# Kernel optimization log

Hardware: AMD Instinct MI355X
Metric: run time of the kernel (lower is better)

Reference implementation:

```python
import jax, jax.numpy as jnp
import numpy as np

B, S, D = 2, 2048, 768
H, DK, DV = 12, 64, 64


def setup_inputs() -> dict:
    key = jax.random.key(0)
    ks = jax.random.split(key, 12)
    sc = 0.02
    return {
        'q': jax.random.normal(ks[0], (B, S, D), jnp.float32),
        'k': jax.random.normal(ks[1], (B, S, D), jnp.float32),
        'v': jax.random.normal(ks[2], (B, S, D), jnp.float32),
        'mask': jnp.zeros((B, H, S, S), jnp.float32),
        'Wq': jax.random.normal(ks[3], (D, H * DK), jnp.float32) * sc,
        'bq': jnp.zeros((H * DK,), jnp.float32),
        'Wk': jax.random.normal(ks[4], (D, H * DK), jnp.float32) * sc,
        'bk': jnp.zeros((H * DK,), jnp.float32),
        'Wv': jax.random.normal(ks[5], (D, H * DV), jnp.float32) * sc,
        'bv': jnp.zeros((H * DV,), jnp.float32),
        'Wo': jax.random.normal(ks[6], (H * DV, D), jnp.float32) * sc,
        'bo': jnp.zeros((D,), jnp.float32),
    }


def reference(q, k, v, mask, Wq, bq, Wk, bk, Wv, bv, Wo, bo):
    b, s, _ = q.shape
    # projections -> [B, H, S, Dk/Dv]
    Q = (q @ Wq + bq).reshape(b, s, H, DK).transpose(0, 2, 1, 3)
    K = (k @ Wk + bk).reshape(b, s, H, DK).transpose(0, 2, 1, 3)
    V = (v @ Wv + bv).reshape(b, s, H, DV).transpose(0, 2, 1, 3)
    scale = 1.0 / np.sqrt(DK).astype(np.float32)
    scores = jnp.einsum('bhqd,bhkd->bhqk', Q, K) * scale + mask
    attn = jax.nn.softmax(scores, axis=-1)  # dropout rate 0.0 -> identity
    ctx = jnp.einsum('bhqk,bhkd->bhqd', attn, V)
    ctx = ctx.transpose(0, 2, 1, 3).reshape(b, s, H * DV)
    out = ctx @ Wo + bo
    return out, attn
```

## Files before the change

kernel.cpp:

```cpp
#include <hip/hip_runtime.h>
#include <hip/hip_bf16.h>

typedef unsigned short u16;
typedef __attribute__((ext_vector_type(8))) short s16x8;
typedef __attribute__((ext_vector_type(4))) float f32x4;

#define MFMA16(a, b, c) __builtin_amdgcn_mfma_f32_16x16x32_bf16((a), (b), (c), 0, 0, 0)

__device__ __forceinline__ float b2f(u16 u) {
    union { float f; unsigned int i; } c; c.i = ((unsigned int)u) << 16; return c.f;
}
__device__ __forceinline__ u16 f2b(float f) {
    union { float f; unsigned int i; } c; c.f = f;
    unsigned int i = c.i;
    return (u16)((i + 0x7fffu + ((i >> 16) & 1u)) >> 16);
}

__device__ __forceinline__ s16x8 load8b(const void* base, size_t idx, int isf32) {
    if (!isf32) {
        return *(const s16x8*)((const u16*)base + idx);
    } else {
        const float* p = (const float*)base + idx;
        f32x4 a = *(const f32x4*)p;
        f32x4 b = *(const f32x4*)(p + 4);
        s16x8 v;
        v[0] = (short)f2b(a[0]); v[1] = (short)f2b(a[1]);
        v[2] = (short)f2b(a[2]); v[3] = (short)f2b(a[3]);
        v[4] = (short)f2b(b[0]); v[5] = (short)f2b(b[1]);
        v[6] = (short)f2b(b[2]); v[7] = (short)f2b(b[3]);
        return v;
    }
}
__device__ __forceinline__ float loadsc(const void* base, size_t idx, int isf32) {
    return isf32 ? ((const float*)base)[idx] : b2f(((const u16*)base)[idx]);
}
__device__ __forceinline__ void load8f_nt(const void* base, size_t idx, int isf32, float* o) {
    if (!isf32) {
        s16x8 m = __builtin_nontemporal_load((const s16x8*)((const u16*)base + idx));
#pragma unroll
        for (int j = 0; j < 8; j++) o[j] = b2f((u16)m[j]);
    } else {
        const float* p = (const float*)base + idx;
        f32x4 a = __builtin_nontemporal_load((const f32x4*)p);
        f32x4 b = __builtin_nontemporal_load((const f32x4*)(p + 4));
        o[0] = a[0]; o[1] = a[1]; o[2] = a[2]; o[3] = a[3];
        o[4] = b[0]; o[5] = b[1]; o[6] = b[2]; o[7] = b[3];
    }
}

__global__ __launch_bounds__(64) void k_detect(const u16* __restrict__ q, int* __restrict__ flag) {
    int t = threadIdx.x;
    int cnt = 0;
#pragma unroll
    for (int i = 0; i < 16; i++) {
        u16 u = q[t * 16 + i];
        int e = (u >> 7) & 0xFF;
        cnt += (e >= 110 && e <= 135) ? 1 : 0;
    }
#pragma unroll
    for (int off = 32; off > 0; off >>= 1) cnt += __shfl_down(cnt, off);
    if (t == 0) *flag = (cnt < 850) ? 1 : 0;
}

__global__ __launch_bounds__(256) void k_transpose(
    const void* __restrict__ w0, const void* __restrict__ w1,
    const void* __restrict__ w2, const void* __restrict__ w3,
    u16* __restrict__ wt, const int* __restrict__ flag)
{
    __shared__ __align__(16) u16 T[64 * 65];
    const int isf32 = *flag;
    const int z = blockIdx.z;
    const void* W = (z == 0) ? w0 : (z == 1) ? w1 : (z == 2) ? w2 : w3;
    u16* WT = wt + (size_t)z * 589824;
    const int n0 = blockIdx.x * 64, k0 = blockIdx.y * 64;
    const int t = threadIdx.x;
    const int r = t >> 3, c = (t & 7) * 8;
    for (int rr = r; rr < 64; rr += 32) {
        s16x8 v = load8b(W, (size_t)(k0 + rr) * 768 + n0 + c, isf32);
#pragma unroll
        for (int j = 0; j < 8; j++) T[(c + j) * 65 + rr] = (u16)v[j];
    }
    __syncthreads();
    const int n = t >> 3, kc = (t & 7) * 8;
    for (int nn = n; nn < 64; nn += 32) {
        s16x8 v;
#pragma unroll
        for (int j = 0; j < 8; j++) v[j] = (short)T[nn * 65 + kc + j];
        *(s16x8*)&WT[(size_t)(n0 + nn) * 768 + k0 + kc] = v;
    }
}

__device__ __forceinline__ void gemm_body(
    const void* __restrict__ A, int a_isf32, const u16* __restrict__ WT,
    const void* __restrict__ bias, int b_isf32, void* __restrict__ out,
    int out_isf32, int epi, int head, int m0)
{
    __shared__ __align__(16) u16 As[128 * 72];
    __shared__ __align__(16) u16 Bs[64 * 72];
    const int t = threadIdx.x;
    const int lane = t & 63, wave = t >> 6;
    const int quad = lane >> 4, l16 = lane & 15;
    const int mrow_base = (wave >> 1) * 64;
    const int ncol_base = (wave & 1) * 32;
    const int hbase = head * 64;

    f32x4 acc[4][2];
#pragma unroll
    for (int mt = 0; mt < 4; mt++)
#pragma unroll
        for (int nt = 0; nt < 2; nt++) acc[mt][nt] = (f32x4){0.f, 0.f, 0.f, 0.f};

    for (int k0 = 0; k0 < 768; k0 += 64) {
#pragma unroll
        for (int i = 0; i < 4; i++) {
            int seg = t + 256 * i;
            int r = seg >> 3, c = (seg & 7) * 8;
            *(s16x8*)&As[r * 72 + c] = load8b(A, (size_t)(m0 + r) * 768 + k0 + c, a_isf32);
        }
#pragma unroll
        for (int i = 0; i < 2; i++) {
            int seg = t + 256 * i;
            int r = seg >> 3, c = (seg & 7) * 8;
            *(s16x8*)&Bs[r * 72 + c] = *(const s16x8*)&WT[(size_t)(hbase + r) * 768 + k0 + c];
        }
        __syncthreads();
#pragma unroll
        for (int ks = 0; ks < 2; ks++) {
            s16x8 af[4], bf[2];
#pragma unroll
            for (int mt = 0; mt < 4; mt++)
                af[mt] = *(const s16x8*)&As[(mrow_base + mt * 16 + l16) * 72 + ks * 32 + quad * 8];
#pragma unroll
            for (int nt = 0; nt < 2; nt++)
                bf[nt] = *(const s16x8*)&Bs[(ncol_base + nt * 16 + l16) * 72 + ks * 32 + quad * 8];
#pragma unroll
            for (int mt = 0; mt < 4; mt++)
#pragma unroll
                for (int nt = 0; nt < 2; nt++)
                    acc[mt][nt] = MFMA16(af[mt], bf[nt], acc[mt][nt]);
        }
        __syncthreads();
    }

    if (epi == 2) {
#pragma unroll
        for (int mt = 0; mt < 4; mt++)
#pragma unroll
            for (int nt = 0; nt < 2; nt++) {
                int nc = ncol_base + nt * 16 + l16;
                float bvv = loadsc(bias, hbase + nc, b_isf32);
#pragma unroll
                for (int r = 0; r < 4; r++) {
                    int m = m0 + mrow_base + mt * 16 + quad * 4 + r;
                    float val = acc[mt][nt][r] + bvv;
                    size_t idx = (size_t)m * 768 + hbase + nc;
                    if (out_isf32) ((float*)out)[idx] = val;
                    else           ((u16*)out)[idx] = f2b(val);
                }
            }
    } else if (epi == 0) {
        u16* ob = (u16*)out;
#pragma unroll
        for (int mt = 0; mt < 4; mt++)
#pragma unroll
            for (int nt = 0; nt < 2; nt++) {
                int nc = ncol_base + nt * 16 + l16;
                float bvv = loadsc(bias, hbase + nc, b_isf32);
#pragma unroll
                for (int r = 0; r < 4; r++) {
                    int m = m0 + mrow_base + mt * 16 + quad * 4 + r;
                    int bidx = m >> 11, s = m & 2047;
                    ob[(((size_t)bidx * 12 + head) * 2048 + s) * 64 + nc] =
                        f2b(acc[mt][nt][r] + bvv);
                }
            }
    } else {
        u16* ob = (u16*)out;
        u16* Ts = As;
#pragma unroll
        for (int mt = 0; mt < 4; mt++)
#pragma unroll
            for (int nt = 0; nt < 2; nt++) {
                int nc = ncol_base + nt * 16 + l16;
                float bvv = loadsc(bias, hbase + nc, b_isf32);
#pragma unroll
                for (int r = 0; r < 4; r++) {
                    int ml = mrow_base + mt * 16 + quad * 4 + r;
                    Ts[nc * 136 + ml] = f2b(acc[mt][nt][r] + bvv);
                }
            }
        __syncthreads();
        const int bidx = m0 >> 11, sbase = m0 & 2047;
#pragma unroll
        for (int i = 0; i < 4; i++) {
            int seg = t + 256 * i;
            int dv = seg >> 4, scc = (seg & 15) * 8;
            s16x8 vv = *(const s16x8*)&Ts[dv * 136 + scc];
            *(s16x8*)&ob[(((size_t)bidx * 12 + head) * 64 + dv) * 2048 + sbase + scc] = vv;
        }
    }
}

__global__ __launch_bounds__(256) void k_qkv(
    const void* __restrict__ q, const void* __restrict__ k, const void* __restrict__ v,
    const u16* __restrict__ wt,
    const void* __restrict__ bq, const void* __restrict__ bk, const void* __restrict__ bv,
    u16* __restrict__ Q, u16* __restrict__ K, u16* __restrict__ Vt,
    const int* __restrict__ flag)
{
    const int isf32 = *flag;
    const int z = blockIdx.z;
    const void* A = (z == 0) ? q : (z == 1) ? k : v;
    const u16* WTz = wt + (size_t)z * 589824;
    const void* bias = (z == 0) ? bq : (z == 1) ? bk : bv;
    u16* out = (z == 0) ? Q : (z == 1) ? K : Vt;
    gemm_body(A, isf32, WTz, bias, isf32, out, 0, (z == 2) ? 1 : 0, blockIdx.y, blockIdx.x * 128);
}

__global__ __launch_bounds__(256) void k_oproj(
    const u16* __restrict__ ctx, const u16* __restrict__ wto,
    const void* __restrict__ bo, void* __restrict__ out,
    const int* __restrict__ flag)
{
    const int isf32 = *flag;
    gemm_body(ctx, 0, wto, bo, isf32, out, isf32, 2, blockIdx.y, blockIdx.x * 128);
}

__device__ __forceinline__ int sw_off(int row, int col) {
    int unit = col >> 3;
    int slot = (unit + row) & 7;
    return row * 2048 + (((unit & ~7) | slot) << 3) + (col & 7);
}

__global__ __launch_bounds__(512, 4) void k_attn(
    const u16* __restrict__ Q, const u16* __restrict__ K,
    const u16* __restrict__ Vt, const void* __restrict__ mask,
    void* __restrict__ outbase, u16* __restrict__ ctx,
    const int* __restrict__ flag)
{
    __shared__ __align__(16) u16 sc[16 * 2048];
    __shared__ __align__(16) float part[1024];
    __shared__ float invs[16];
    const int isf32 = *flag;
    const int t = threadIdx.x;
    const int lane = t & 63, wave = t >> 6;
    const int quad = lane >> 4, l16 = lane & 15;
    const int q0 = blockIdx.x * 16;
    const int h = blockIdx.y, b = blockIdx.z;
    const int bh = b * 12 + h;

    const u16* Qb = Q + ((size_t)bh * 2048 + q0) * 64;
    const s16x8 qf0 = *(const s16x8*)&Qb[l16 * 64 + quad * 8];
    const s16x8 qf1 = *(const s16x8*)&Qb[l16 * 64 + 32 + quad * 8];

    const u16* Kb = K + (size_t)bh * 2048 * 64;
    const size_t mrow0 = ((size_t)bh * 2048 + q0) * 2048;

#pragma unroll 4
    for (int it = 0; it < 16; it++) {
        const int kc = it * 128 + wave * 16;
        const u16* kp = &Kb[(size_t)(kc + l16) * 64 + quad * 8];
        s16x8 kf0 = *(const s16x8*)kp;
        s16x8 kf1 = *(const s16x8*)(kp + 32);
        f32x4 a = (f32x4){0.f, 0.f, 0.f, 0.f};
        a = MFMA16(qf0, kf0, a);
        a = MFMA16(qf1, kf1, a);
        const int col = kc + l16;
#pragma unroll
        for (int r = 0; r < 4; r++)
            sc[sw_off(quad * 4 + r, col)] = f2b(a[r] * 0.125f);
    }
    __syncthreads();

    const int row = t >> 5, j32 = t & 31;
    float mx = -3.4e38f;
#pragma unroll 4
    for (int i = 0; i < 8; i++) {
        const int c0 = j32 * 8 + i * 256;
        float mk[8];
        load8f_nt(mask, mrow0 + (size_t)row * 2048 + c0, isf32, mk);
        s16x8* sp = (s16x8*)&sc[sw_off(row, c0)];
        s16x8 sv = *sp, nv;
#pragma unroll
        for (int j = 0; j < 8; j++) {
            float x = b2f((u16)sv[j]) + mk[j];
            nv[j] = (short)f2b(x);
            mx = fmaxf(mx, x);
        }
        *sp = nv;
    }
#pragma unroll
    for (int off = 16; off > 0; off >>= 1) mx = fmaxf(mx, __shfl_xor(mx, off));

    float sum = 0.f;
#pragma unroll 4
    for (int i = 0; i < 8; i++) {
        const int c0 = j32 * 8 + i * 256;
        s16x8* sp = (s16x8*)&sc[sw_off(row, c0)];
        s16x8 sv = *sp, nv;
#pragma unroll
        for (int j = 0; j < 8; j++) {
            float e = __expf(b2f((u16)sv[j]) - mx);
            nv[j] = (short)f2b(e);
            sum += e;
        }
        *sp = nv;
    }
#pragma unroll
    for (int off = 16; off > 0; off >>= 1) sum += __shfl_xor(sum, off);
    const float inv = 1.0f / sum;
    if (j32 == 0) invs[row] = inv;

    const size_t aoff = 3145728 + mrow0 + (size_t)row * 2048;
#pragma unroll 2
    for (int i = 0; i < 8; i++) {
        const int c0 = j32 * 8 + i * 256;
        s16x8 sv = *(const s16x8*)&sc[sw_off(row, c0)];
        if (isf32) {
            float* arow = (float*)outbase + aoff;
            f32x4 lo, hi;
#pragma unroll
            for (int j = 0; j < 4; j++) lo[j] = b2f((u16)sv[j]) * inv;
#pragma unroll
            for (int j = 0; j < 4; j++) hi[j] = b2f((u16)sv[j + 4]) * inv;
            *(f32x4*)&arow[c0] = lo;
            *(f32x4*)&arow[c0 + 4] = hi;
        } else {
            u16* arow = (u16*)outbase + aoff;
            s16x8 pv;
#pragma unroll
            for (int j = 0; j < 8; j++) pv[j] = (short)f2b(b2f((u16)sv[j]) * inv);
            *(s16x8*)&arow[c0] = pv;
        }
    }
    __syncthreads();

    const int wg = wave >> 2;
    const int dv = (wave & 3) * 16 + l16;
    const u16* vrow = Vt + ((size_t)bh * 64 + dv) * 2048;
    f32x4 o = (f32x4){0.f, 0.f, 0.f, 0.f};
    const int kbase = wg * 32;
#pragma unroll 4
    for (int kk = 0; kk < 32; kk++) {
        const int kcol = (kbase + kk) * 32 + quad * 8;
        s16x8 pa = *(const s16x8*)&sc[sw_off(l16, kcol)];
        s16x8 vb = *(const s16x8*)&vrow[kcol];
        o = MFMA16(pa, vb, o);
    }
    if (wg == 1) *(f32x4*)&part[((wave & 3) * 64 + lane) * 4] = o;
    __syncthreads();
    if (wg == 0) {
        f32x4 o2 = *(const f32x4*)&part[((wave & 3) * 64 + lane) * 4];
#pragma unroll
        for (int r = 0; r < 4; r++) {
            float val = (o[r] + o2[r]) * invs[quad * 4 + r];
            ctx[((size_t)b * 2048 + q0 + quad * 4 + r) * 768 + h * 64 + dv] = f2b(val);
        }
    }
}

extern "C" void kernel_launch(void* const* d_in, const int* in_sizes, int n_in,
                              void* d_out, int out_size, void* d_ws, size_t ws_size,
                              hipStream_t stream) {
    const void* q    = d_in[0];
    const void* k    = d_in[1];
    const void* v    = d_in[2];
    const void* mask = d_in[3];
    const void* Wq   = d_in[4];
    const void* bq   = d_in[5];
    const void* Wk   = d_in[6];
    const void* bk   = d_in[7];
    const void* Wv   = d_in[8];
    const void* bv   = d_in[9];
    const void* Wo   = d_in[10];
    const void* bo   = d_in[11];

    u16* ws  = (u16*)d_ws;
    u16* WT  = ws;
    u16* Qb  = ws + 2359296;
    u16* Kb  = ws + 5505024;
    u16* Vtb = ws + 8650752;
    u16* ctx = ws + 11796480;
    int* flag = (int*)(ws + 14942208);

    k_detect<<<1, 64, 0, stream>>>((const u16*)q, flag);
    k_transpose<<<dim3(12, 12, 4), 256, 0, stream>>>(Wq, Wk, Wv, Wo, WT, flag);
    k_qkv<<<dim3(32, 12, 3), 256, 0, stream>>>(q, k, v, WT, bq, bk, bv, Qb, Kb, Vtb, flag);
    k_attn<<<dim3(128, 12, 2), 512, 0, stream>>>(Qb, Kb, Vtb, mask, d_out, ctx, flag);
    k_oproj<<<dim3(32, 12, 1), 256, 0, stream>>>(ctx, WT + 3 * 589824, bo, d_out, flag);
}
```

Before: 924.3 us.

## Pre-convert QKV inputs to bf16, prefetch mask early, defer attn store

Adds a conversion kernel that turns the fp32 q/k/v activations into bf16 buffers in workspace before the projection GEMM, so the GEMM streams half-width operands. It is used only when the workspace is large enough. In the attention kernel, the mask rows are loaded into registers at kernel start so their latency overlaps the QK^T MFMA phase, and the softmax pass keeps masked scores in registers instead of writing them back to LDS. The normalized attention-probability store moves after the PV computation so it overlaps with compute. The trade-offs are an extra launch and an extra pass over q/k/v, plus 64 more live registers per thread, which may lower occupancy.

```diff
diff --git a/kernel.cpp b/kernel.cpp
--- a/kernel.cpp
+++ b/kernel.cpp
@@ -62,6 +62,20 @@
     if (t == 0) *flag = (cnt < 850) ? 1 : 0;
 }
 
+__global__ __launch_bounds__(256) void k_cvt(
+    const void* __restrict__ q, const void* __restrict__ k, const void* __restrict__ v,
+    u16* __restrict__ Qc, u16* __restrict__ Kc, u16* __restrict__ Vc,
+    const int* __restrict__ flag)
+{
+    const int isf32 = *flag;
+    const int z = blockIdx.y;
+    const void* src = (z == 0) ? q : (z == 1) ? k : v;
+    u16* dst = (z == 0) ? Qc : (z == 1) ? Kc : Vc;
+    size_t idx = ((size_t)blockIdx.x * 256 + threadIdx.x) * 8;
+    s16x8 vv = load8b(src, idx, isf32);
+    *(s16x8*)&dst[idx] = vv;
+}
+
 __global__ __launch_bounds__(256) void k_transpose(
     const void* __restrict__ w0, const void* __restrict__ w1,
     const void* __restrict__ w2, const void* __restrict__ w3,
@@ -206,7 +220,7 @@
     const u16* __restrict__ wt,
     const void* __restrict__ bq, const void* __restrict__ bk, const void* __restrict__ bv,
     u16* __restrict__ Q, u16* __restrict__ K, u16* __restrict__ Vt,
-    const int* __restrict__ flag)
+    const int* __restrict__ flag, int use_cvt)
 {
     const int isf32 = *flag;
     const int z = blockIdx.z;
@@ -214,7 +228,8 @@
     const u16* WTz = wt + (size_t)z * 589824;
     const void* bias = (z == 0) ? bq : (z == 1) ? bk : bv;
     u16* out = (z == 0) ? Q : (z == 1) ? K : Vt;
-    gemm_body(A, isf32, WTz, bias, isf32, out, 0, (z == 2) ? 1 : 0, blockIdx.y, blockIdx.x * 128);
+    gemm_body(A, use_cvt ? 0 : isf32, WTz, bias, isf32, out, 0,
+              (z == 2) ? 1 : 0, blockIdx.y, blockIdx.x * 128);
 }
 
 __global__ __launch_bounds__(256) void k_oproj(
@@ -248,13 +263,18 @@
     const int q0 = blockIdx.x * 16;
     const int h = blockIdx.y, b = blockIdx.z;
     const int bh = b * 12 + h;
+    const size_t mrow0 = ((size_t)bh * 2048 + q0) * 2048;
+    const int row = t >> 5, j32 = t & 31;
+
+    float mk[8][8];
+#pragma unroll
+    for (int i = 0; i < 8; i++)
+        load8f_nt(mask, mrow0 + (size_t)row * 2048 + j32 * 8 + i * 256, isf32, mk[i]);
 
     const u16* Qb = Q + ((size_t)bh * 2048 + q0) * 64;
     const s16x8 qf0 = *(const s16x8*)&Qb[l16 * 64 + quad * 8];
     const s16x8 qf1 = *(const s16x8*)&Qb[l16 * 64 + 32 + quad * 8];
-
     const u16* Kb = K + (size_t)bh * 2048 * 64;
-    const size_t mrow0 = ((size_t)bh * 2048 + q0) * 2048;
 
 #pragma unroll 4
     for (int it = 0; it < 16; it++) {
@@ -272,67 +292,37 @@
     }
     __syncthreads();
 
-    const int row = t >> 5, j32 = t & 31;
     float mx = -3.4e38f;
-#pragma unroll 4
+#pragma unroll
     for (int i = 0; i < 8; i++) {
         const int c0 = j32 * 8 + i * 256;
-        float mk[8];
-        load8f_nt(mask, mrow0 + (size_t)row * 2048 + c0, isf32, mk);
-        s16x8* sp = (s16x8*)&sc[sw_off(row, c0)];
-        s16x8 sv = *sp, nv;
+        s16x8 sv = *(const s16x8*)&sc[sw_off(row, c0)];
 #pragma unroll
         for (int j = 0; j < 8; j++) {
-            float x = b2f((u16)sv[j]) + mk[j];
-            nv[j] = (short)f2b(x);
-            mx = fmaxf(mx, x);
-        }
-        *sp = nv;
+            mk[i][j] += b2f((u16)sv[j]);
+            mx = fmaxf(mx, mk[i][j]);
+        }
     }
 #pragma unroll
     for (int off = 16; off > 0; off >>= 1) mx = fmaxf(mx, __shfl_xor(mx, off));
 
     float sum = 0.f;
-#pragma unroll 4
+#pragma unroll
     for (int i = 0; i < 8; i++) {
         const int c0 = j32 * 8 + i * 256;
-        s16x8* sp = (s16x8*)&sc[sw_off(row, c0)];
-        s16x8 sv = *sp, nv;
+        s16x8 nv;
 #pragma unroll
         for (int j = 0; j < 8; j++) {
-            float e = __expf(b2f((u16)sv[j]) - mx);
+            float e = __expf(mk[i][j] - mx);
             nv[j] = (short)f2b(e);
             sum += e;
         }
-        *sp = nv;
+        *(s16x8*)&sc[sw_off(row, c0)] = nv;
     }
 #pragma unroll
     for (int off = 16; off > 0; off >>= 1) sum += __shfl_xor(sum, off);
     const float inv = 1.0f / sum;
     if (j32 == 0) invs[row] = inv;
-
-    const size_t aoff = 3145728 + mrow0 + (size_t)row * 2048;
-#pragma unroll 2
-    for (int i = 0; i < 8; i++) {
-        const int c0 = j32 * 8 + i * 256;
-        s16x8 sv = *(const s16x8*)&sc[sw_off(row, c0)];
-        if (isf32) {
-            float* arow = (float*)outbase + aoff;
-            f32x4 lo, hi;
-#pragma unroll
-            for (int j = 0; j < 4; j++) lo[j] = b2f((u16)sv[j]) * inv;
-#pragma unroll
-            for (int j = 0; j < 4; j++) hi[j] = b2f((u16)sv[j + 4]) * inv;
-            *(f32x4*)&arow[c0] = lo;
-            *(f32x4*)&arow[c0 + 4] = hi;
-        } else {
-            u16* arow = (u16*)outbase + aoff;
-            s16x8 pv;
-#pragma unroll
-            for (int j = 0; j < 8; j++) pv[j] = (short)f2b(b2f((u16)sv[j]) * inv);
-            *(s16x8*)&arow[c0] = pv;
-        }
-    }
     __syncthreads();
 
     const int wg = wave >> 2;
@@ -355,6 +345,29 @@
         for (int r = 0; r < 4; r++) {
             float val = (o[r] + o2[r]) * invs[quad * 4 + r];
             ctx[((size_t)b * 2048 + q0 + quad * 4 + r) * 768 + h * 64 + dv] = f2b(val);
+        }
+    }
+
+    const size_t aoff = 3145728 + mrow0 + (size_t)row * 2048;
+#pragma unroll 2
+    for (int i = 0; i < 8; i++) {
+        const int c0 = j32 * 8 + i * 256;
+        s16x8 sv = *(const s16x8*)&sc[sw_off(row, c0)];
+        if (isf32) {
+            float* arow = (float*)outbase + aoff;
+            f32x4 lo, hi;
+#pragma unroll
+            for (int j = 0; j < 4; j++) lo[j] = b2f((u16)sv[j]) * inv;
+#pragma unroll
+            for (int j = 0; j < 4; j++) hi[j] = b2f((u16)sv[j + 4]) * inv;
+            *(f32x4*)&arow[c0] = lo;
+            *(f32x4*)&arow[c0 + 4] = hi;
+        } else {
+            u16* arow = (u16*)outbase + aoff;
+            s16x8 pv;
+#pragma unroll
+            for (int j = 0; j < 8; j++) pv[j] = (short)f2b(b2f((u16)sv[j]) * inv);
+            *(s16x8*)&arow[c0] = pv;
         }
     }
 }
@@ -383,9 +396,21 @@
     u16* ctx = ws + 11796480;
     int* flag = (int*)(ws + 14942208);
 
+    u16* Qc = ws + 14942224;
+    u16* Kc = Qc + 3145728;
+    u16* Vc = Kc + 3145728;
+    const int use_cvt = (ws_size >= (size_t)48758816) ? 1 : 0;
+
     k_detect<<<1, 64, 0, stream>>>((const u16*)q, flag);
     k_transpose<<<dim3(12, 12, 4), 256, 0, stream>>>(Wq, Wk, Wv, Wo, WT, flag);
-    k_qkv<<<dim3(32, 12, 3), 256, 0, stream>>>(q, k, v, WT, bq, bk, bv, Qb, Kb, Vtb, flag);
+    if (use_cvt) {
+        k_cvt<<<dim3(1536, 3), 256, 0, stream>>>(q, k, v, Qc, Kc, Vc, flag);
+        k_qkv<<<dim3(32, 12, 3), 256, 0, stream>>>(Qc, Kc, Vc, WT, bq, bk, bv,
+                                                   Qb, Kb, Vtb, flag, 1);
+    } else {
+        k_qkv<<<dim3(32, 12, 3), 256, 0, stream>>>(q, k, v, WT, bq, bk, bv,
+                                                   Qb, Kb, Vtb, flag, 0);
+    }
     k_attn<<<dim3(128, 12, 2), 512, 0, stream>>>(Qb, Kb, Vtb, mask, d_out, ctx, flag);
     k_oproj<<<dim3(32, 12, 1), 256, 0, stream>>>(ctx, WT + 3 * 589824, bo, d_out, flag);
 }
```

Result: faster. 902.6 us (-2.3%).
